# Optimization experiments

Measured on AMD Instinct MI355X. Metric: run time of the kernel, lower is better.

Reference implementation:

```python
import jax, jax.numpy as jnp
import numpy as np

E, H = 512, 256  # embed_dim, hidden_dim
B, SQ, SK = 2, 512, 512


def _linear_params(k, fin, fout):
    lim = 1.0 / np.sqrt(fin)
    kw, kb = jax.random.split(k)
    W = jax.random.uniform(kw, (fin, fout), minval=-lim, maxval=lim, dtype=jnp.float32)
    b = jax.random.uniform(kb, (fout,), minval=-lim, maxval=lim, dtype=jnp.float32)
    return W, b


def setup_inputs() -> dict:
    rng = jax.random.key(0)
    ks = jax.random.split(rng, 12)
    query = jax.random.normal(ks[0], (B, SQ, E), dtype=jnp.float32)
    key = jax.random.normal(ks[1], (B, SK, E), dtype=jnp.float32)
    Wqe, bqe = _linear_params(ks[2], E, H)
    Wke, bke = _linear_params(ks[3], E, H)
    W1, b1 = _linear_params(ks[4], 2 * H, H)  # importance_predictor layer 0
    W2, b2 = _linear_params(ks[5], H, H)      # layer 1
    W3, b3 = _linear_params(ks[6], H, H)      # layer 2
    Wf, bf = _linear_params(ks[7], H, 1)      # final importance logit
    Wv1, bv1 = _linear_params(ks[8], 2 * H, H)  # variance_estimator layer 0
    Wv2, bv2 = _linear_params(ks[9], H, 1)      # variance_estimator final
    return {"query": query, "key": key,
            "Wqe": Wqe, "bqe": bqe, "Wke": Wke, "bke": bke,
            "W1": W1, "b1": b1, "W2": W2, "b2": b2, "W3": W3, "b3": b3,
            "Wf": Wf, "bf": bf, "Wv1": Wv1, "bv1": bv1, "Wv2": Wv2, "bv2": bv2}


def reference(query, key, Wqe, bqe, Wke, bke, W1, b1, W2, b2, W3, b3, Wf, bf, Wv1, bv1, Wv2, bv2):
    # Encoders (dropout is identity at eval)
    qf = jax.nn.relu(jnp.einsum('bqe,eh->bqh', query, Wqe) + bqe)  # [B,Sq,H]
    kf = jax.nn.relu(jnp.einsum('bke,eh->bkh', key, Wke) + bke)    # [B,Sk,H]

    # First Linear(2H,H) on cat([q,k]) == q@W1[:H] + k@W1[H:]; broadcast over pairs
    qp = jnp.einsum('bqh,hd->bqd', qf, W1[:H])
    kp = jnp.einsum('bkh,hd->bkd', kf, W1[H:])
    h = jax.nn.relu(qp[:, :, None, :] + kp[:, None, :, :] + b1)  # [B,Sq,Sk,H]
    h = jax.nn.relu(jnp.einsum('bqkh,hd->bqkd', h, W2) + b2)
    h = jax.nn.relu(jnp.einsum('bqkh,hd->bqkd', h, W3) + b3)
    importance_logits = (jnp.einsum('bqkh,ho->bqko', h, Wf) + bf)[..., 0]  # [B,Sq,Sk]

    # Variance head: Linear(2H,H) split the same way, ReLU, Linear, Softplus
    vq = jnp.einsum('bqh,hd->bqd', qf, Wv1[:H])
    vk = jnp.einsum('bkh,hd->bkd', kf, Wv1[H:])
    v = jax.nn.relu(vq[:, :, None, :] + vk[:, None, :, :] + bv1)  # [B,Sq,Sk,H]
    estimated_variance = jax.nn.softplus((jnp.einsum('bqkh,ho->bqko', v, Wv2) + bv2)[..., 0])
    return importance_logits, estimated_variance
```

## Files before the change

kernel.cpp:

```cpp
#include <hip/hip_runtime.h>
#include <hip/hip_bf16.h>
#include <cstdint>
#include <cstddef>
#include <cstring>

#define HDIM 256
#define EDIM 512
#define NB   2
#define NSQ  512
#define NSK  512

typedef _Float16 f16x8 __attribute__((ext_vector_type(8)));
typedef _Float16 h2    __attribute__((ext_vector_type(2)));
typedef __fp16   fp16v2 __attribute__((ext_vector_type(2)));
typedef float    f32x4  __attribute__((ext_vector_type(4)));

#define OFF_W2F  0u
#define OFF_W3F  65536u
#define OFF_WQEF 131072u
#define OFF_WKEF 262144u
#define OFF_WCQ  393216u
#define OFF_WCK  524288u
#define OFF_WV2H 655360u
#define F16_WS_END_BYTES 1312768u

union U8 { f16x8 v; h2 h[4]; };

__device__ __forceinline__ ushort2 f2h2(float x, float y) {
  fp16v2 r = __builtin_amdgcn_cvt_pkrtz(x, y);
  ushort2 u;
  __builtin_memcpy(&u, &r, 4);
  return u;
}
__device__ __forceinline__ float relu_(float x) { return x > 0.f ? x : 0.f; }
__device__ __forceinline__ float softplus_(float x) {
  return fmaxf(x, 0.f) + log1pf(expf(-fabsf(x)));
}

__global__ __launch_bounds__(256) void shuffle_weights(
    const float* __restrict__ Wqe, const float* __restrict__ Wke,
    const float* __restrict__ W1,  const float* __restrict__ Wv1,
    const float* __restrict__ W2,  const float* __restrict__ W3,
    const float* __restrict__ Wv2,
    unsigned short* __restrict__ wsb)
{
  __shared__ float sW[32 * 257];
  const int bx = blockIdx.x;
  const int t = threadIdx.x;
  if (bx == 80) {
    if (t < 64) {
      float a = Wv2[t * 4 + 0], b = Wv2[t * 4 + 1];
      float c = Wv2[t * 4 + 2], d = Wv2[t * 4 + 3];
      ushort2 lo = f2h2(a, b), hi = f2h2(c, d);
      ushort4 o; o.x = lo.x; o.y = lo.y; o.z = hi.x; o.w = hi.y;
      *(ushort4*)&wsb[OFF_WV2H + t * 4] = o;
    }
    return;
  }
  const float* src; unsigned short* dst; int s; int S;
  if      (bx <  8) { src = W2;          dst = wsb + OFF_W2F;           s = bx;      S = 8;  }
  else if (bx < 16) { src = W3;          dst = wsb + OFF_W3F;           s = bx - 8;  S = 8;  }
  else if (bx < 32) { src = Wqe;         dst = wsb + OFF_WQEF;          s = bx - 16; S = 16; }
  else if (bx < 48) { src = Wke;         dst = wsb + OFF_WKEF;          s = bx - 32; S = 16; }
  else if (bx < 56) { src = W1;          dst = wsb + OFF_WCQ;           s = bx - 48; S = 8;  }
  else if (bx < 64) { src = Wv1;         dst = wsb + OFF_WCQ + 65536u;  s = bx - 56; S = 8;  }
  else if (bx < 72) { src = W1 + 65536;  dst = wsb + OFF_WCK;           s = bx - 64; S = 8;  }
  else              { src = Wv1 + 65536; dst = wsb + OFF_WCK + 65536u;  s = bx - 72; S = 8;  }

  const int kbase = s * 32;
  #pragma unroll
  for (int it = 0; it < 8; ++it) {
    const int f4 = it * 256 + t;
    const int row = f4 >> 6, c4 = (f4 & 63) * 4;
    float4 v = *(const float4*)(src + (size_t)(kbase + row) * 256 + c4);
    sW[row * 257 + c4 + 0] = v.x; sW[row * 257 + c4 + 1] = v.y;
    sW[row * 257 + c4 + 2] = v.z; sW[row * 257 + c4 + 3] = v.w;
  }
  __syncthreads();

  const int wave = t >> 6, lane = t & 63;
  const int n_in = lane & 15, k0 = (lane >> 4) * 8;
  for (int tt = wave * 4; tt < wave * 4 + 4; ++tt) {
    const int n = tt * 16 + n_in;
    float x[8];
    #pragma unroll
    for (int j = 0; j < 8; ++j) x[j] = sW[(k0 + j) * 257 + n];
    ushort2 p0 = f2h2(x[0], x[1]), p1 = f2h2(x[2], x[3]);
    ushort2 p2 = f2h2(x[4], x[5]), p3 = f2h2(x[6], x[7]);
    ushort4 lo; lo.x = p0.x; lo.y = p0.y; lo.z = p1.x; lo.w = p1.y;
    ushort4 hi; hi.x = p2.x; hi.y = p2.y; hi.z = p3.x; hi.w = p3.y;
    unsigned short* o = dst + ((size_t)(tt * S + s) * 64 + lane) * 8;
    *(ushort4*)&o[0] = lo; *(ushort4*)&o[4] = hi;
  }
}

__global__ __launch_bounds__(256) void encoder_kernel(
    const float* __restrict__ query, const float* __restrict__ key,
    const float* __restrict__ bqe,   const float* __restrict__ bke,
    const float* __restrict__ b1,    const float* __restrict__ bv1,
    const unsigned short* __restrict__ WqeF, const unsigned short* __restrict__ WkeF,
    const unsigned short* __restrict__ WcqF, const unsigned short* __restrict__ WckF,
    _Float16* __restrict__ Pq, _Float16* __restrict__ Pk)
{
  __shared__ unsigned short sX[16 * 520];
  __shared__ unsigned short sF[16 * 264];
  __shared__ float sBe[256];
  __shared__ float sBc[512];

  const int bx   = blockIdx.x;
  const int side = bx >> 6;
  const int rt   = bx & 63;
  const int t    = threadIdx.x;

  const float* Xsrc = side ? key : query;
  const unsigned short* WeF = side ? WkeF : WqeF;
  const unsigned short* WcF = side ? WckF : WcqF;
  _Float16* P = side ? Pk : Pq;

  {
    const int m = t >> 4, ch = t & 15;
    const float* xr = Xsrc + (size_t)(rt * 16 + m) * EDIM;
    #pragma unroll
    for (int j = 0; j < 4; ++j) {
      const int c = ch * 32 + j * 8;
      float4 v0 = *(const float4*)(xr + c);
      float4 v1 = *(const float4*)(xr + c + 4);
      ushort2 p0 = f2h2(v0.x, v0.y), p1 = f2h2(v0.z, v0.w);
      ushort2 p2 = f2h2(v1.x, v1.y), p3 = f2h2(v1.z, v1.w);
      ushort4 lo; lo.x = p0.x; lo.y = p0.y; lo.z = p1.x; lo.w = p1.y;
      ushort4 hi; hi.x = p2.x; hi.y = p2.y; hi.z = p3.x; hi.w = p3.y;
      *(ushort4*)&sX[m * 520 + c] = lo;
      *(ushort4*)&sX[m * 520 + c + 4] = hi;
    }
    sBe[t]       = side ? bke[t] : bqe[t];
    sBc[t]       = side ? 0.f : b1[t];
    sBc[256 + t] = side ? 0.f : bv1[t];
  }
  __syncthreads();

  const int wave = t >> 6, lane = t & 63;
  const int l15 = lane & 15, q4 = lane >> 4;

  f32x4 acc1[4];
  #pragma unroll
  for (int ft = 0; ft < 4; ++ft) acc1[ft] = (f32x4){0.f, 0.f, 0.f, 0.f};

  for (int s = 0; s < 16; ++s) {
    f16x8 af[4], bfr;
    #pragma unroll
    for (int ft = 0; ft < 4; ++ft) {
      const int tg = wave * 4 + ft;
      af[ft] = *(const f16x8*)(WeF + ((size_t)(tg * 16 + s) * 64 + lane) * 8);
    }
    bfr = *(const f16x8*)&sX[l15 * 520 + s * 32 + q4 * 8];
    #pragma unroll
    for (int ft = 0; ft < 4; ++ft)
      acc1[ft] = __builtin_amdgcn_mfma_f32_16x16x32_f16(af[ft], bfr, acc1[ft], 0, 0, 0);
  }

  #pragma unroll
  for (int ft = 0; ft < 4; ++ft) {
    const int tg = wave * 4 + ft;
    const int n0 = tg * 16 + q4 * 4;
    float4 b4 = *(const float4*)&sBe[n0];
    f32x4 a = acc1[ft];
    ushort2 lo = f2h2(relu_(a[0] + b4.x), relu_(a[1] + b4.y));
    ushort2 hi = f2h2(relu_(a[2] + b4.z), relu_(a[3] + b4.w));
    ushort4 h; h.x = lo.x; h.y = lo.y; h.z = hi.x; h.w = hi.y;
    *(ushort4*)&sF[l15 * 264 + n0] = h;
  }
  __syncthreads();

  f32x4 acc2[8];
  #pragma unroll
  for (int ft = 0; ft < 8; ++ft) acc2[ft] = (f32x4){0.f, 0.f, 0.f, 0.f};

  for (int s = 0; s < 8; ++s) {
    f16x8 af[8], bfr;
    #pragma unroll
    for (int ft = 0; ft < 8; ++ft) {
      const int tg = wave * 8 + ft;
      af[ft] = *(const f16x8*)(WcF + ((size_t)(tg * 8 + s) * 64 + lane) * 8);
    }
    bfr = *(const f16x8*)&sF[l15 * 264 + s * 32 + q4 * 8];
    #pragma unroll
    for (int ft = 0; ft < 8; ++ft)
      acc2[ft] = __builtin_amdgcn_mfma_f32_16x16x32_f16(af[ft], bfr, acc2[ft], 0, 0, 0);
  }

  #pragma unroll
  for (int ft = 0; ft < 8; ++ft) {
    const int tg = wave * 8 + ft;
    const int n0 = tg * 16 + q4 * 4;
    float4 bc = *(const float4*)&sBc[n0];
    const int row = rt * 16 + l15;
    f32x4 a = acc2[ft];
    ushort2 lo = f2h2(a[0] + bc.x, a[1] + bc.y);
    ushort2 hi = f2h2(a[2] + bc.z, a[3] + bc.w);
    ushort4 o; o.x = lo.x; o.y = lo.y; o.z = hi.x; o.w = hi.y;
    *(ushort4*)((unsigned short*)P + (size_t)row * 512 + n0) = o;
  }
}

__global__ __launch_bounds__(512, 4) void pair_kernel(
    const _Float16* __restrict__ Pq, const _Float16* __restrict__ Pk,
    const unsigned short* __restrict__ W2F, const unsigned short* __restrict__ W3F,
    const float* __restrict__ b2, const float* __restrict__ b3,
    const float* __restrict__ Wf, const float* __restrict__ bfp,
    const unsigned short* __restrict__ Wv2H, const float* __restrict__ bv2p,
    float* __restrict__ out)
{
  __shared__ __align__(16) unsigned char smem[36864];
  unsigned short* sXH = (unsigned short*)smem;
  float* sB2  = (float*)(smem + 33792);
  float* sB3  = (float*)(smem + 34816);
  float* sWf  = (float*)(smem + 35840);
  float* sRed = (float*)(smem + 33792);

  const int kt = blockIdx.x, qy = blockIdx.y, bz = blockIdx.z;
  const int t = threadIdx.x;
  const _Float16* qpRow = Pq + (size_t)(bz * NSQ + qy) * 512;

  const int wave = t >> 6, lane = t & 63;
  const int l15 = lane & 15, q4 = lane >> 4;
  const int nq = wave & 3, mi = wave >> 2;

  const unsigned short* a2base = W2F + ((size_t)(nq * 4) * 8 * 64 + lane) * 8;
  const unsigned short* a3base = W3F + ((size_t)(nq * 4) * 8 * 64 + lane) * 8;

  f16x8 afd[2][4];
  #pragma unroll
  for (int ft = 0; ft < 4; ++ft)
    afd[0][ft] = *(const f16x8*)(a2base + ft * 4096);

  {
    const int m   = t >> 3;
    const int sub = t & 7;
    const _Float16* kpRow = Pk + (size_t)(bz * NSK + kt * 64 + m) * 512;
    const f16x8 z8 = {0, 0, 0, 0, 0, 0, 0, 0};
    float vpart = 0.f;
    #pragma unroll
    for (int it = 0; it < 4; ++it) {
      const int c = it * 64 + sub * 8;
      f16x8 q8 = *(const f16x8*)(qpRow + c);
      f16x8 k8 = *(const f16x8*)(kpRow + c);
      f16x8 r  = __builtin_elementwise_max(q8 + k8, z8);
      *(f16x8*)&sXH[m * 264 + c] = r;
      f16x8 a8 = *(const f16x8*)(qpRow + 256 + c);
      f16x8 v8 = *(const f16x8*)(kpRow + 256 + c);
      U8 ar; ar.v = __builtin_elementwise_max(a8 + v8, z8);
      U8 w8; w8.v = *(const f16x8*)((const _Float16*)Wv2H + c);
      vpart = __builtin_amdgcn_fdot2(ar.h[0], w8.h[0], vpart, false);
      vpart = __builtin_amdgcn_fdot2(ar.h[1], w8.h[1], vpart, false);
      vpart = __builtin_amdgcn_fdot2(ar.h[2], w8.h[2], vpart, false);
      vpart = __builtin_amdgcn_fdot2(ar.h[3], w8.h[3], vpart, false);
    }
    vpart += __shfl_xor(vpart, 1, 64);
    vpart += __shfl_xor(vpart, 2, 64);
    vpart += __shfl_xor(vpart, 4, 64);
    if (sub == 0) {
      const size_t o = (size_t)(bz * NSQ + qy) * NSK + kt * 64 + m;
      out[(size_t)NB * NSQ * NSK + o] = softplus_(vpart + bv2p[0]);
    }
    if (t < 256) { sB2[t] = b2[t]; sB3[t] = b3[t]; sWf[t] = Wf[t]; }
  }
  __syncthreads();

  f32x4 acc[4][2];
  #pragma unroll
  for (int ft = 0; ft < 4; ++ft)
    #pragma unroll
    for (int pt = 0; pt < 2; ++pt)
      acc[ft][pt] = (f32x4){0.f, 0.f, 0.f, 0.f};

  #pragma unroll
  for (int s = 0; s < 8; ++s) {
    if (s < 7) {
      #pragma unroll
      for (int ft = 0; ft < 4; ++ft)
        afd[(s + 1) & 1][ft] = *(const f16x8*)(a2base + ft * 4096 + (size_t)(s + 1) * 512);
    }
    f16x8 bfr[2];
    #pragma unroll
    for (int pt = 0; pt < 2; ++pt)
      bfr[pt] = *(const f16x8*)&sXH[(mi * 32 + pt * 16 + l15) * 264 + s * 32 + q4 * 8];
    #pragma unroll
    for (int ft = 0; ft < 4; ++ft)
      #pragma unroll
      for (int pt = 0; pt < 2; ++pt)
        acc[ft][pt] = __builtin_amdgcn_mfma_f32_16x16x32_f16(afd[s & 1][ft], bfr[pt], acc[ft][pt], 0, 0, 0);
  }
  __syncthreads();

  #pragma unroll
  for (int ft = 0; ft < 4; ++ft)
    afd[0][ft] = *(const f16x8*)(a3base + ft * 4096);

  #pragma unroll
  for (int ft = 0; ft < 4; ++ft) {
    const int n0 = (nq * 4 + ft) * 16 + q4 * 4;
    float4 b4 = *(const float4*)&sB2[n0];
    #pragma unroll
    for (int pt = 0; pt < 2; ++pt) {
      const int mr = mi * 32 + pt * 16 + l15;
      f32x4 a = acc[ft][pt];
      ushort2 lo = f2h2(relu_(a[0] + b4.x), relu_(a[1] + b4.y));
      ushort2 hi = f2h2(relu_(a[2] + b4.z), relu_(a[3] + b4.w));
      ushort4 h; h.x = lo.x; h.y = lo.y; h.z = hi.x; h.w = hi.y;
      *(ushort4*)&sXH[mr * 264 + n0] = h;
    }
  }
  __syncthreads();

  f32x4 acc2[4][2];
  #pragma unroll
  for (int ft = 0; ft < 4; ++ft)
    #pragma unroll
    for (int pt = 0; pt < 2; ++pt)
      acc2[ft][pt] = (f32x4){0.f, 0.f, 0.f, 0.f};

  #pragma unroll
  for (int s = 0; s < 8; ++s) {
    if (s < 7) {
      #pragma unroll
      for (int ft = 0; ft < 4; ++ft)
        afd[(s + 1) & 1][ft] = *(const f16x8*)(a3base + ft * 4096 + (size_t)(s + 1) * 512);
    }
    f16x8 bfr[2];
    #pragma unroll
    for (int pt = 0; pt < 2; ++pt)
      bfr[pt] = *(const f16x8*)&sXH[(mi * 32 + pt * 16 + l15) * 264 + s * 32 + q4 * 8];
    #pragma unroll
    for (int ft = 0; ft < 4; ++ft)
      #pragma unroll
      for (int pt = 0; pt < 2; ++pt)
        acc2[ft][pt] = __builtin_amdgcn_mfma_f32_16x16x32_f16(afd[s & 1][ft], bfr[pt], acc2[ft][pt], 0, 0, 0);
  }

  float p[2] = {0.f, 0.f};
  #pragma unroll
  for (int ft = 0; ft < 4; ++ft) {
    const int n0 = (nq * 4 + ft) * 16 + q4 * 4;
    float4 b4 = *(const float4*)&sB3[n0];
    float4 w4 = *(const float4*)&sWf[n0];
    #pragma unroll
    for (int pt = 0; pt < 2; ++pt) {
      f32x4 a = acc2[ft][pt];
      p[pt] += relu_(a[0] + b4.x) * w4.x + relu_(a[1] + b4.y) * w4.y
             + relu_(a[2] + b4.z) * w4.z + relu_(a[3] + b4.w) * w4.w;
    }
  }
  __syncthreads();
  #pragma unroll
  for (int pt = 0; pt < 2; ++pt) {
    float v = p[pt];
    v += __shfl_xor(v, 16, 64);
    v += __shfl_xor(v, 32, 64);
    if (lane < 16) sRed[wave * 32 + pt * 16 + lane] = v;
  }
  __syncthreads();

  if (t < 64) {
    const size_t o = (size_t)(bz * NSQ + qy) * NSK + kt * 64 + t;
    const int mh = t >> 5, rel = t & 31;
    float lg = bfp[0];
    #pragma unroll
    for (int j = 0; j < 4; ++j) lg += sRed[(mh * 4 + j) * 32 + rel];
    out[o] = lg;
  }
}

extern "C" void kernel_launch(void* const* d_in, const int* in_sizes, int n_in,
                              void* d_out, int out_size, void* d_ws, size_t ws_size,
                              hipStream_t stream)
{
  (void)in_sizes; (void)n_in; (void)out_size; (void)ws_size;
  const float* query = (const float*)d_in[0];
  const float* key   = (const float*)d_in[1];
  const float* Wqe   = (const float*)d_in[2];
  const float* bqe   = (const float*)d_in[3];
  const float* Wke   = (const float*)d_in[4];
  const float* bke   = (const float*)d_in[5];
  const float* W1    = (const float*)d_in[6];
  const float* b1    = (const float*)d_in[7];
  const float* W2    = (const float*)d_in[8];
  const float* b2    = (const float*)d_in[9];
  const float* W3    = (const float*)d_in[10];
  const float* b3    = (const float*)d_in[11];
  const float* Wf    = (const float*)d_in[12];
  const float* bf    = (const float*)d_in[13];
  const float* Wv1   = (const float*)d_in[14];
  const float* bv1   = (const float*)d_in[15];
  const float* Wv2   = (const float*)d_in[16];
  const float* bv2   = (const float*)d_in[17];

  unsigned short* wsb = (unsigned short*)d_ws;
  _Float16* Pq = (_Float16*)((char*)d_ws + F16_WS_END_BYTES);
  _Float16* Pk = Pq + (size_t)1024 * 512;
  float* out = (float*)d_out;

  shuffle_weights<<<81, 256, 0, stream>>>(Wqe, Wke, W1, Wv1, W2, W3, Wv2, wsb);
  encoder_kernel<<<128, 256, 0, stream>>>(query, key, bqe, bke, b1, bv1,
      wsb + OFF_WQEF, wsb + OFF_WKEF, wsb + OFF_WCQ, wsb + OFF_WCK, Pq, Pk);
  pair_kernel<<<dim3(NSK / 64, NSQ, NB), 512, 0, stream>>>(Pq, Pk,
      wsb + OFF_W2F, wsb + OFF_W3F, b2, b3, Wf, bf, wsb + OFF_WV2H, bv2, out);
}
```

Before: 290.4 us.

## Shrink pair kernel to 4 waves covering all 64 rows, split encoder output columns

The pair kernel drops from 512 to 256 threads. Each wave now computes all 64 pair rows for its 64 output features, so every A-fragment of W2/W3 loaded from global memory feeds twice as many MFMAs and the block's weight traffic is halved. In exchange each wave holds more accumulator registers, and the launch-bounds occupancy hint is removed. The encoder kernel splits its second GEMM's output columns across two blocks, giving 256 blocks instead of 128, and both of its GEMM loops now double-buffer their weight-fragment loads so global latency overlaps the MFMAs.

```diff
diff --git a/kernel.cpp b/kernel.cpp
--- a/kernel.cpp
+++ b/kernel.cpp
@@ -108,8 +108,10 @@
   __shared__ float sBc[512];
 
   const int bx   = blockIdx.x;
-  const int side = bx >> 6;
-  const int rt   = bx & 63;
+  const int side = bx >> 7;
+  const int idx  = bx & 127;
+  const int rt   = idx >> 1;
+  const int nh   = idx & 1;
   const int t    = threadIdx.x;
 
   const float* Xsrc = side ? key : query;
@@ -136,26 +138,33 @@
     sBc[t]       = side ? 0.f : b1[t];
     sBc[256 + t] = side ? 0.f : bv1[t];
   }
-  __syncthreads();
 
   const int wave = t >> 6, lane = t & 63;
   const int l15 = lane & 15, q4 = lane >> 4;
 
+  const unsigned short* aeb = WeF + ((size_t)(wave * 4) * 16 * 64 + lane) * 8;
+  f16x8 afe[2][4];
+  #pragma unroll
+  for (int ft = 0; ft < 4; ++ft)
+    afe[0][ft] = *(const f16x8*)(aeb + ft * 8192);
+
+  __syncthreads();
+
   f32x4 acc1[4];
   #pragma unroll
   for (int ft = 0; ft < 4; ++ft) acc1[ft] = (f32x4){0.f, 0.f, 0.f, 0.f};
 
+  #pragma unroll
   for (int s = 0; s < 16; ++s) {
-    f16x8 af[4], bfr;
-    #pragma unroll
-    for (int ft = 0; ft < 4; ++ft) {
-      const int tg = wave * 4 + ft;
-      af[ft] = *(const f16x8*)(WeF + ((size_t)(tg * 16 + s) * 64 + lane) * 8);
-    }
-    bfr = *(const f16x8*)&sX[l15 * 520 + s * 32 + q4 * 8];
+    if (s < 15) {
+      #pragma unroll
+      for (int ft = 0; ft < 4; ++ft)
+        afe[(s + 1) & 1][ft] = *(const f16x8*)(aeb + ft * 8192 + (size_t)(s + 1) * 512);
+    }
+    f16x8 bfr = *(const f16x8*)&sX[l15 * 520 + s * 32 + q4 * 8];
     #pragma unroll
     for (int ft = 0; ft < 4; ++ft)
-      acc1[ft] = __builtin_amdgcn_mfma_f32_16x16x32_f16(af[ft], bfr, acc1[ft], 0, 0, 0);
+      acc1[ft] = __builtin_amdgcn_mfma_f32_16x16x32_f16(afe[s & 1][ft], bfr, acc1[ft], 0, 0, 0);
   }
 
   #pragma unroll
@@ -171,26 +180,32 @@
   }
   __syncthreads();
 
-  f32x4 acc2[8];
-  #pragma unroll
-  for (int ft = 0; ft < 8; ++ft) acc2[ft] = (f32x4){0.f, 0.f, 0.f, 0.f};
-
+  const unsigned short* acb = WcF + ((size_t)(nh * 16 + wave * 4) * 8 * 64 + lane) * 8;
+  f16x8 afc[2][4];
+  #pragma unroll
+  for (int ft = 0; ft < 4; ++ft)
+    afc[0][ft] = *(const f16x8*)(acb + ft * 4096);
+
+  f32x4 acc2[4];
+  #pragma unroll
+  for (int ft = 0; ft < 4; ++ft) acc2[ft] = (f32x4){0.f, 0.f, 0.f, 0.f};
+
+  #pragma unroll
   for (int s = 0; s < 8; ++s) {
-    f16x8 af[8], bfr;
-    #pragma unroll
-    for (int ft = 0; ft < 8; ++ft) {
-      const int tg = wave * 8 + ft;
-      af[ft] = *(const f16x8*)(WcF + ((size_t)(tg * 8 + s) * 64 + lane) * 8);
-    }
-    bfr = *(const f16x8*)&sF[l15 * 264 + s * 32 + q4 * 8];
-    #pragma unroll
-    for (int ft = 0; ft < 8; ++ft)
-      acc2[ft] = __builtin_amdgcn_mfma_f32_16x16x32_f16(af[ft], bfr, acc2[ft], 0, 0, 0);
-  }
-
-  #pragma unroll
-  for (int ft = 0; ft < 8; ++ft) {
-    const int tg = wave * 8 + ft;
+    if (s < 7) {
+      #pragma unroll
+      for (int ft = 0; ft < 4; ++ft)
+        afc[(s + 1) & 1][ft] = *(const f16x8*)(acb + ft * 4096 + (size_t)(s + 1) * 512);
+    }
+    f16x8 bfr = *(const f16x8*)&sF[l15 * 264 + s * 32 + q4 * 8];
+    #pragma unroll
+    for (int ft = 0; ft < 4; ++ft)
+      acc2[ft] = __builtin_amdgcn_mfma_f32_16x16x32_f16(afc[s & 1][ft], bfr, acc2[ft], 0, 0, 0);
+  }
+
+  #pragma unroll
+  for (int ft = 0; ft < 4; ++ft) {
+    const int tg = nh * 16 + wave * 4 + ft;
     const int n0 = tg * 16 + q4 * 4;
     float4 bc = *(const float4*)&sBc[n0];
     const int row = rt * 16 + l15;
@@ -202,7 +217,7 @@
   }
 }
 
-__global__ __launch_bounds__(512, 4) void pair_kernel(
+__global__ __launch_bounds__(256) void pair_kernel(
     const _Float16* __restrict__ Pq, const _Float16* __restrict__ Pk,
     const unsigned short* __restrict__ W2F, const unsigned short* __restrict__ W3F,
     const float* __restrict__ b2, const float* __restrict__ b3,
@@ -223,10 +238,9 @@
 
   const int wave = t >> 6, lane = t & 63;
   const int l15 = lane & 15, q4 = lane >> 4;
-  const int nq = wave & 3, mi = wave >> 2;
-
-  const unsigned short* a2base = W2F + ((size_t)(nq * 4) * 8 * 64 + lane) * 8;
-  const unsigned short* a3base = W3F + ((size_t)(nq * 4) * 8 * 64 + lane) * 8;
+
+  const unsigned short* a2base = W2F + ((size_t)(wave * 4) * 8 * 64 + lane) * 8;
+  const unsigned short* a3base = W3F + ((size_t)(wave * 4) * 8 * 64 + lane) * 8;
 
   f16x8 afd[2][4];
   #pragma unroll
@@ -234,14 +248,14 @@
     afd[0][ft] = *(const f16x8*)(a2base + ft * 4096);
 
   {
-    const int m   = t >> 3;
-    const int sub = t & 7;
+    const int m   = t >> 2;
+    const int sub = t & 3;
     const _Float16* kpRow = Pk + (size_t)(bz * NSK + kt * 64 + m) * 512;
     const f16x8 z8 = {0, 0, 0, 0, 0, 0, 0, 0};
     float vpart = 0.f;
     #pragma unroll
-    for (int it = 0; it < 4; ++it) {
-      const int c = it * 64 + sub * 8;
+    for (int it = 0; it < 8; ++it) {
+      const int c = sub * 64 + it * 8;
       f16x8 q8 = *(const f16x8*)(qpRow + c);
       f16x8 k8 = *(const f16x8*)(kpRow + c);
       f16x8 r  = __builtin_elementwise_max(q8 + k8, z8);
@@ -257,20 +271,19 @@
     }
     vpart += __shfl_xor(vpart, 1, 64);
     vpart += __shfl_xor(vpart, 2, 64);
-    vpart += __shfl_xor(vpart, 4, 64);
     if (sub == 0) {
       const size_t o = (size_t)(bz * NSQ + qy) * NSK + kt * 64 + m;
       out[(size_t)NB * NSQ * NSK + o] = softplus_(vpart + bv2p[0]);
     }
-    if (t < 256) { sB2[t] = b2[t]; sB3[t] = b3[t]; sWf[t] = Wf[t]; }
-  }
-  __syncthreads();
-
-  f32x4 acc[4][2];
-  #pragma unroll
-  for (int ft = 0; ft < 4; ++ft)
-    #pragma unroll
-    for (int pt = 0; pt < 2; ++pt)
+    sB2[t] = b2[t]; sB3[t] = b3[t]; sWf[t] = Wf[t];
+  }
+  __syncthreads();
+
+  f32x4 acc[4][4];
+  #pragma unroll
+  for (int ft = 0; ft < 4; ++ft)
+    #pragma unroll
+    for (int pt = 0; pt < 4; ++pt)
       acc[ft][pt] = (f32x4){0.f, 0.f, 0.f, 0.f};
 
   #pragma unroll
@@ -280,14 +293,14 @@
       for (int ft = 0; ft < 4; ++ft)
         afd[(s + 1) & 1][ft] = *(const f16x8*)(a2base + ft * 4096 + (size_t)(s + 1) * 512);
     }
-    f16x8 bfr[2];
-    #pragma unroll
-    for (int pt = 0; pt < 2; ++pt)
-      bfr[pt] = *(const f16x8*)&sXH[(mi * 32 + pt * 16 + l15) * 264 + s * 32 + q4 * 8];
+    f16x8 bfr[4];
+    #pragma unroll
+    for (int pt = 0; pt < 4; ++pt)
+      bfr[pt] = *(const f16x8*)&sXH[(pt * 16 + l15) * 264 + s * 32 + q4 * 8];
     #pragma unroll
     for (int ft = 0; ft < 4; ++ft)
       #pragma unroll
-      for (int pt = 0; pt < 2; ++pt)
+      for (int pt = 0; pt < 4; ++pt)
         acc[ft][pt] = __builtin_amdgcn_mfma_f32_16x16x32_f16(afd[s & 1][ft], bfr[pt], acc[ft][pt], 0, 0, 0);
   }
   __syncthreads();
@@ -298,11 +311,11 @@
 
   #pragma unroll
   for (int ft = 0; ft < 4; ++ft) {
-    const int n0 = (nq * 4 + ft) * 16 + q4 * 4;
+    const int n0 = (wave * 4 + ft) * 16 + q4 * 4;
     float4 b4 = *(const float4*)&sB2[n0];
     #pragma unroll
-    for (int pt = 0; pt < 2; ++pt) {
-      const int mr = mi * 32 + pt * 16 + l15;
+    for (int pt = 0; pt < 4; ++pt) {
+      const int mr = pt * 16 + l15;
       f32x4 a = acc[ft][pt];
       ushort2 lo = f2h2(relu_(a[0] + b4.x), relu_(a[1] + b4.y));
       ushort2 hi = f2h2(relu_(a[2] + b4.z), relu_(a[3] + b4.w));
@@ -312,11 +325,11 @@
   }
   __syncthreads();
 
-  f32x4 acc2[4][2];
-  #pragma unroll
-  for (int ft = 0; ft < 4; ++ft)
-    #pragma unroll
-    for (int pt = 0; pt < 2; ++pt)
+  f32x4 acc2[4][4];
+  #pragma unroll
+  for (int ft = 0; ft < 4; ++ft)
+    #pragma unroll
+    for (int pt = 0; pt < 4; ++pt)
       acc2[ft][pt] = (f32x4){0.f, 0.f, 0.f, 0.f};
 
   #pragma unroll
@@ -326,46 +339,42 @@
       for (int ft = 0; ft < 4; ++ft)
         afd[(s + 1) & 1][ft] = *(const f16x8*)(a3base + ft * 4096 + (size_t)(s + 1) * 512);
     }
-    f16x8 bfr[2];
-    #pragma unroll
-    for (int pt = 0; pt < 2; ++pt)
-      bfr[pt] = *(const f16x8*)&sXH[(mi * 32 + pt * 16 + l15) * 264 + s * 32 + q4 * 8];
+    f16x8 bfr[4];
+    #pragma unroll
+    for (int pt = 0; pt < 4; ++pt)
+      bfr[pt] = *(const f16x8*)&sXH[(pt * 16 + l15) * 264 + s * 32 + q4 * 8];
     #pragma unroll
     for (int ft = 0; ft < 4; ++ft)
       #pragma unroll
-      for (int pt = 0; pt < 2; ++pt)
+      for (int pt = 0; pt < 4; ++pt)
         acc2[ft][pt] = __builtin_amdgcn_mfma_f32_16x16x32_f16(afd[s & 1][ft], bfr[pt], acc2[ft][pt], 0, 0, 0);
   }
 
-  float p[2] = {0.f, 0.f};
+  float p[4] = {0.f, 0.f, 0.f, 0.f};
   #pragma unroll
   for (int ft = 0; ft < 4; ++ft) {
-    const int n0 = (nq * 4 + ft) * 16 + q4 * 4;
+    const int n0 = (wave * 4 + ft) * 16 + q4 * 4;
     float4 b4 = *(const float4*)&sB3[n0];
     float4 w4 = *(const float4*)&sWf[n0];
     #pragma unroll
-    for (int pt = 0; pt < 2; ++pt) {
+    for (int pt = 0; pt < 4; ++pt) {
       f32x4 a = acc2[ft][pt];
       p[pt] += relu_(a[0] + b4.x) * w4.x + relu_(a[1] + b4.y) * w4.y
              + relu_(a[2] + b4.z) * w4.z + relu_(a[3] + b4.w) * w4.w;
     }
   }
-  __syncthreads();
-  #pragma unroll
-  for (int pt = 0; pt < 2; ++pt) {
+  #pragma unroll
+  for (int pt = 0; pt < 4; ++pt) {
     float v = p[pt];
     v += __shfl_xor(v, 16, 64);
     v += __shfl_xor(v, 32, 64);
-    if (lane < 16) sRed[wave * 32 + pt * 16 + lane] = v;
+    if (lane < 16) sRed[wave * 64 + pt * 16 + lane] = v;
   }
   __syncthreads();
 
   if (t < 64) {
     const size_t o = (size_t)(bz * NSQ + qy) * NSK + kt * 64 + t;
-    const int mh = t >> 5, rel = t & 31;
-    float lg = bfp[0];
-    #pragma unroll
-    for (int j = 0; j < 4; ++j) lg += sRed[(mh * 4 + j) * 32 + rel];
+    float lg = bfp[0] + sRed[t] + sRed[64 + t] + sRed[128 + t] + sRed[192 + t];
     out[o] = lg;
   }
 }
@@ -400,8 +409,8 @@
   float* out = (float*)d_out;
 
   shuffle_weights<<<81, 256, 0, stream>>>(Wqe, Wke, W1, Wv1, W2, W3, Wv2, wsb);
-  encoder_kernel<<<128, 256, 0, stream>>>(query, key, bqe, bke, b1, bv1,
+  encoder_kernel<<<256, 256, 0, stream>>>(query, key, bqe, bke, b1, bv1,
       wsb + OFF_WQEF, wsb + OFF_WKEF, wsb + OFF_WCQ, wsb + OFF_WCK, Pq, Pk);
-  pair_kernel<<<dim3(NSK / 64, NSQ, NB), 512, 0, stream>>>(Pq, Pk,
+  pair_kernel<<<dim3(NSK / 64, NSQ, NB), 256, 0, stream>>>(Pq, Pk,
       wsb + OFF_W2F, wsb + OFF_W3F, b2, b3, Wf, bf, wsb + OFF_WV2H, bv2, out);
 }
```

After: 340.3 us. 17.2% more time.
